# Performance work log

Measured on AMD Instinct MI355X. Metric: run time of the kernel, lower is better.

Reference implementation:

```python
import jax, jax.numpy as jnp
import numpy as np

D = 16          # u_emb_size
LAYER_NUM = 2   # CAN layer_num

def setup_inputs() -> dict:
    key = jax.random.key(0)
    k1, k2 = jax.random.split(key)
    B, N = 16384, 50
    user_emb = jax.random.normal(k1, (B, N, D), dtype=jnp.float32)
    # item side packs per-sample MLP params: [W0(d*d), b0(d), W1(d*d), b1(d)]
    item_emb = jax.random.normal(k2, (B, D * (D + 1) * LAYER_NUM), dtype=jnp.float32)
    return {"user_emb": user_emb, "item_emb": item_emb}

def reference(user_emb, item_emb):
    B = user_emb.shape[0]
    x = user_emb  # (B, N, D)
    off = 0
    for _ in range(LAYER_NUM):
        W = item_emb[:, off:off + D * D].reshape(B, D, D); off += D * D
        b = item_emb[:, off:off + D].reshape(B, 1, D);      off += D
        # per-sample batched matmul + bias + relu
        x = jax.nn.relu(jnp.einsum('bnd,bde->bne', x, W) + b)
    return x  # (B, N, D); is_seq=False, is_stacked=True -> return as-is
```

## Files before the change

kernel.cpp:

```cpp
#include <hip/hip_runtime.h>


#define CAN_D 16
#define CAN_N 50
#define CAN_PSTRIDE 544
#define WAVES_PER_BLOCK 4
#define YSTRIDE 20

typedef __attribute__((ext_vector_type(8))) short short8;
typedef __attribute__((ext_vector_type(4))) float f32x4;

union ABFrag { int i[4]; short8 v; };

__device__ __forceinline__ int pack2(float lo, float hi) {
    unsigned short ua = __builtin_bit_cast(unsigned short, (__bf16)lo);
    unsigned short ub = __builtin_bit_cast(unsigned short, (__bf16)hi);
    return (int)((unsigned)ua | ((unsigned)ub << 16));
}

__global__ __launch_bounds__(256, 5) void can_kernel(
    const float* __restrict__ user_emb,
    const float* __restrict__ item_emb,
    float* __restrict__ out, int B)
{
    __shared__ __align__(16) float ybuf[WAVES_PER_BLOCK][2][16 * YSTRIDE];

    const int wave = threadIdx.x >> 6;
    const int lane = threadIdx.x & 63;
    const int s = blockIdx.x * WAVES_PER_BLOCK + wave;
    if (s >= B) return;

    const int n    = lane & 15;
    const int quad = lane >> 4;

    const float* __restrict__ P     = item_emb + (size_t)s * CAN_PSTRIDE;
    const float* __restrict__ xbase = user_emb + (size_t)s * (CAN_N * CAN_D);
    float* __restrict__ obase       = out      + (size_t)s * (CAN_N * CAN_D);

    float t0[8], t1[8];
    if (quad < 2) {
        const float* W0 = P + quad * 8 * CAN_D + n;
        const float* W1 = P + 272 + quad * 8 * CAN_D + n;
#pragma unroll
        for (int j = 0; j < 8; ++j) { t0[j] = W0[j * CAN_D]; t1[j] = W1[j * CAN_D]; }
    }
    const float b0v = P[256 + n];
    const float b1v = P[528 + n];

    float4 xu0[4], xu1[4];
#pragma unroll
    for (int t = 0; t < 4; ++t) {
        if (quad < 2) {
            int row = t * 16 + n;
            if (row > CAN_N - 1) row = CAN_N - 1;
            const float4* px = (const float4*)(xbase + row * CAN_D + quad * 8);
            xu0[t] = px[0];
            xu1[t] = px[1];
        }
    }

    ABFrag w0, w1;
    if (quad < 2) {
#pragma unroll
        for (int j = 0; j < 4; ++j) {
            w0.i[j] = pack2(t0[2 * j], t0[2 * j + 1]);
            w1.i[j] = pack2(t1[2 * j], t1[2 * j + 1]);
        }
    } else {
#pragma unroll
        for (int j = 0; j < 4; ++j) { w0.i[j] = 0; w1.i[j] = 0; }
    }

    ABFrag a0[4];
#pragma unroll
    for (int t = 0; t < 4; ++t) {
        if (quad < 2) {
            a0[t].i[0] = pack2(xu0[t].x, xu0[t].y);
            a0[t].i[1] = pack2(xu0[t].z, xu0[t].w);
            a0[t].i[2] = pack2(xu1[t].x, xu1[t].y);
            a0[t].i[3] = pack2(xu1[t].z, xu1[t].w);
        } else {
#pragma unroll
            for (int j = 0; j < 4; ++j) a0[t].i[j] = 0;
        }
    }

#pragma unroll
    for (int t = 0; t < 4; ++t) {
        float* yb = &ybuf[wave][t & 1][0];

        f32x4 c0 = {b0v, b0v, b0v, b0v};
        c0 = __builtin_amdgcn_mfma_f32_16x16x32_bf16(a0[t].v, w0.v, c0, 0, 0, 0);

#pragma unroll
        for (int r = 0; r < 4; ++r)
            yb[(quad * 4 + r) * YSTRIDE + n] = fmaxf(c0[r], 0.0f);

        ABFrag a1;
        if (quad < 2) {
            const float* pr = yb + n * YSTRIDE + quad * 8;
            float4 v0 = *(const float4*)pr;
            float4 v1 = *(const float4*)(pr + 4);
            a1.i[0] = pack2(v0.x, v0.y);
            a1.i[1] = pack2(v0.z, v0.w);
            a1.i[2] = pack2(v1.x, v1.y);
            a1.i[3] = pack2(v1.z, v1.w);
        } else {
#pragma unroll
            for (int j = 0; j < 4; ++j) a1.i[j] = 0;
        }

        f32x4 c1 = {b1v, b1v, b1v, b1v};
        c1 = __builtin_amdgcn_mfma_f32_16x16x32_bf16(a1.v, w1.v, c1, 0, 0, 0);

#pragma unroll
        for (int r = 0; r < 4; ++r)
            yb[(quad * 4 + r) * YSTRIDE + n] = fmaxf(c1[r], 0.0f);

        const int srow = lane >> 2;
        const int scol = lane & 3;
        float4 ov = *(const float4*)(yb + srow * YSTRIDE + scol * 4);
        const int grow = t * 16 + srow;
        if (grow < CAN_N)
            *(float4*)(obase + grow * CAN_D + scol * 4) = ov;
    }
}

extern "C" void kernel_launch(void* const* d_in, const int* in_sizes, int n_in,
                              void* d_out, int out_size, void* d_ws, size_t ws_size,
                              hipStream_t stream) {
    const float* user_emb = (const float*)d_in[0];
    const float* item_emb = (const float*)d_in[1];
    float* out = (float*)d_out;

    const int B = in_sizes[0] / (CAN_N * CAN_D);
    const int blocks = (B + WAVES_PER_BLOCK - 1) / WAVES_PER_BLOCK;
    can_kernel<<<blocks, 256, 0, stream>>>(user_emb, item_emb, out, B);
}
```

Measured before the change: 126.5 us.

## Stage inputs into LDS with global_load_lds DMA and store outputs directly

Each wave now bulk-copies its sample's user embedding and per-sample MLP parameters from global memory into LDS using global_load_lds, with fully coalesced 16-byte transfers. Operand fragments are then built from LDS instead of through strided per-lane global loads. The layer-1 output is written straight from MFMA accumulators to global memory as 4-byte stores, dropping the LDS transpose. This also reuses the x staging area as the intermediate buffer, which makes LDS use per block larger, adds a block-wide barrier, and leaves the output stores less coalesced.

```diff
diff --git a/kernel.cpp b/kernel.cpp
--- a/kernel.cpp
+++ b/kernel.cpp
@@ -5,10 +5,15 @@
 #define CAN_N 50
 #define CAN_PSTRIDE 544
 #define WAVES_PER_BLOCK 4
-#define YSTRIDE 20
+#define XSTAGE 3328
+#define PSTAGE 2304
+#define SSTAGE (XSTAGE + PSTAGE)
+#define YS 20
 
 typedef __attribute__((ext_vector_type(8))) short short8;
 typedef __attribute__((ext_vector_type(4))) float f32x4;
+#define AS1 __attribute__((address_space(1)))
+#define AS3 __attribute__((address_space(3)))
 
 union ABFrag { int i[4]; short8 v; };
 
@@ -18,49 +23,60 @@
     return (int)((unsigned)ua | ((unsigned)ub << 16));
 }
 
+__device__ __forceinline__ void dma16(const float* g, char* l) {
+    __builtin_amdgcn_global_load_lds((const AS1 void*)g, (AS3 void*)l, 16, 0, 0);
+}
+__device__ __forceinline__ void dma4(const float* g, char* l) {
+    __builtin_amdgcn_global_load_lds((const AS1 void*)g, (AS3 void*)l, 4, 0, 0);
+}
+
 __global__ __launch_bounds__(256, 5) void can_kernel(
     const float* __restrict__ user_emb,
     const float* __restrict__ item_emb,
     float* __restrict__ out, int B)
 {
-    __shared__ __align__(16) float ybuf[WAVES_PER_BLOCK][2][16 * YSTRIDE];
+    __shared__ __align__(16) char smem[WAVES_PER_BLOCK * SSTAGE];
 
     const int wave = threadIdx.x >> 6;
     const int lane = threadIdx.x & 63;
     const int s = blockIdx.x * WAVES_PER_BLOCK + wave;
-    if (s >= B) return;
+    const bool active = (s < B);
+
+    char* xw = smem + wave * SSTAGE;
+    char* pw = xw + XSTAGE;
+
+    if (active) {
+        const float* gx = user_emb + (size_t)s * (CAN_N * CAN_D);
+        const float* gp = item_emb + (size_t)s * CAN_PSTRIDE;
+        dma16(gx +       lane * 4, xw);
+        dma16(gx + 256 + lane * 4, xw + 1024);
+        dma16(gx + 512 + lane * 4, xw + 2048);
+        { int idx = 768 + lane; if (idx > 799) idx = 799;
+          dma4(gx + idx, xw + 3072); }
+        dma16(gp +       lane * 4, pw);
+        dma16(gp + 256 + lane * 4, pw + 1024);
+        { int idx = 512 + lane; if (idx > 543) idx = 543;
+          dma4(gp + idx, pw + 2048); }
+    }
+
+    __syncthreads();
+    if (!active) return;
 
     const int n    = lane & 15;
     const int quad = lane >> 4;
-
-    const float* __restrict__ P     = item_emb + (size_t)s * CAN_PSTRIDE;
-    const float* __restrict__ xbase = user_emb + (size_t)s * (CAN_N * CAN_D);
-    float* __restrict__ obase       = out      + (size_t)s * (CAN_N * CAN_D);
-
-    float t0[8], t1[8];
-    if (quad < 2) {
-        const float* W0 = P + quad * 8 * CAN_D + n;
-        const float* W1 = P + 272 + quad * 8 * CAN_D + n;
-#pragma unroll
-        for (int j = 0; j < 8; ++j) { t0[j] = W0[j * CAN_D]; t1[j] = W1[j * CAN_D]; }
-    }
-    const float b0v = P[256 + n];
-    const float b1v = P[528 + n];
-
-    float4 xu0[4], xu1[4];
-#pragma unroll
-    for (int t = 0; t < 4; ++t) {
-        if (quad < 2) {
-            int row = t * 16 + n;
-            if (row > CAN_N - 1) row = CAN_N - 1;
-            const float4* px = (const float4*)(xbase + row * CAN_D + quad * 8);
-            xu0[t] = px[0];
-            xu1[t] = px[1];
-        }
-    }
+    const float* pf = (const float*)pw;
+    const float* xf = (const float*)xw;
 
     ABFrag w0, w1;
+    const float b0v = pf[256 + n];
+    const float b1v = pf[528 + n];
     if (quad < 2) {
+        float t0[8], t1[8];
+#pragma unroll
+        for (int j = 0; j < 8; ++j) {
+            t0[j] = pf[(quad * 8 + j) * CAN_D + n];
+            t1[j] = pf[272 + (quad * 8 + j) * CAN_D + n];
+        }
 #pragma unroll
         for (int j = 0; j < 4; ++j) {
             w0.i[j] = pack2(t0[2 * j], t0[2 * j + 1]);
@@ -75,30 +91,36 @@
 #pragma unroll
     for (int t = 0; t < 4; ++t) {
         if (quad < 2) {
-            a0[t].i[0] = pack2(xu0[t].x, xu0[t].y);
-            a0[t].i[1] = pack2(xu0[t].z, xu0[t].w);
-            a0[t].i[2] = pack2(xu1[t].x, xu1[t].y);
-            a0[t].i[3] = pack2(xu1[t].z, xu1[t].w);
+            int row = t * 16 + n;
+            if (row > CAN_N - 1) row = CAN_N - 1;
+            const float4* pr = (const float4*)(xf + row * CAN_D + quad * 8);
+            float4 u0 = pr[0], u1 = pr[1];
+            a0[t].i[0] = pack2(u0.x, u0.y);
+            a0[t].i[1] = pack2(u0.z, u0.w);
+            a0[t].i[2] = pack2(u1.x, u1.y);
+            a0[t].i[3] = pack2(u1.z, u1.w);
         } else {
 #pragma unroll
             for (int j = 0; j < 4; ++j) a0[t].i[j] = 0;
         }
     }
 
+    float* ob = out + (size_t)s * (CAN_N * CAN_D);
+
 #pragma unroll
     for (int t = 0; t < 4; ++t) {
-        float* yb = &ybuf[wave][t & 1][0];
+        float* yt = (float*)(xw + (t & 1) * 1280);
 
         f32x4 c0 = {b0v, b0v, b0v, b0v};
         c0 = __builtin_amdgcn_mfma_f32_16x16x32_bf16(a0[t].v, w0.v, c0, 0, 0, 0);
 
 #pragma unroll
         for (int r = 0; r < 4; ++r)
-            yb[(quad * 4 + r) * YSTRIDE + n] = fmaxf(c0[r], 0.0f);
+            yt[(quad * 4 + r) * YS + n] = fmaxf(c0[r], 0.0f);
 
         ABFrag a1;
         if (quad < 2) {
-            const float* pr = yb + n * YSTRIDE + quad * 8;
+            const float* pr = yt + n * YS + quad * 8;
             float4 v0 = *(const float4*)pr;
             float4 v1 = *(const float4*)(pr + 4);
             a1.i[0] = pack2(v0.x, v0.y);
@@ -114,15 +136,11 @@
         c1 = __builtin_amdgcn_mfma_f32_16x16x32_bf16(a1.v, w1.v, c1, 0, 0, 0);
 
 #pragma unroll
-        for (int r = 0; r < 4; ++r)
-            yb[(quad * 4 + r) * YSTRIDE + n] = fmaxf(c1[r], 0.0f);
-
-        const int srow = lane >> 2;
-        const int scol = lane & 3;
-        float4 ov = *(const float4*)(yb + srow * YSTRIDE + scol * 4);
-        const int grow = t * 16 + srow;
-        if (grow < CAN_N)
-            *(float4*)(obase + grow * CAN_D + scol * 4) = ov;
+        for (int r = 0; r < 4; ++r) {
+            int grow = t * 16 + quad * 4 + r;
+            if (grow < CAN_N)
+                ob[grow * CAN_D + n] = fmaxf(c1[r], 0.0f);
+        }
     }
 }
 
```

Result: faster. 124.0 us (-2.0%).

## Transpose MFMA operands and exchange layer activations via ds_bpermute instead of LDS

Applied to the files above, without the earlier changes.

Swaps the A/B operands of the MFMA so each lane's accumulator holds four consecutive output features for one row. Layer-0 results are packed to bf16 and redistributed across lanes with ds_bpermute, removing the shared-memory staging buffer and its store/load round trips. Final outputs are written straight from registers as float4 stores, and biases load as float4. Occupancy hint drops from 5 to 4 blocks, and the user-embedding loads are now interleaved with packing instead of issued all up front, which may reduce memory-level parallelism.

```diff
diff --git a/kernel.cpp b/kernel.cpp
--- a/kernel.cpp
+++ b/kernel.cpp
@@ -5,7 +5,6 @@
 #define CAN_N 50
 #define CAN_PSTRIDE 544
 #define WAVES_PER_BLOCK 4
-#define YSTRIDE 20
 
 typedef __attribute__((ext_vector_type(8))) short short8;
 typedef __attribute__((ext_vector_type(4))) float f32x4;
@@ -18,49 +17,31 @@
     return (int)((unsigned)ua | ((unsigned)ub << 16));
 }
 
-__global__ __launch_bounds__(256, 5) void can_kernel(
+__global__ __launch_bounds__(256, 4) void can_kernel(
     const float* __restrict__ user_emb,
     const float* __restrict__ item_emb,
     float* __restrict__ out, int B)
 {
-    __shared__ __align__(16) float ybuf[WAVES_PER_BLOCK][2][16 * YSTRIDE];
-
     const int wave = threadIdx.x >> 6;
     const int lane = threadIdx.x & 63;
     const int s = blockIdx.x * WAVES_PER_BLOCK + wave;
     if (s >= B) return;
 
-    const int n    = lane & 15;
+    const int e    = lane & 15;
     const int quad = lane >> 4;
 
-    const float* __restrict__ P     = item_emb + (size_t)s * CAN_PSTRIDE;
-    const float* __restrict__ xbase = user_emb + (size_t)s * (CAN_N * CAN_D);
-    float* __restrict__ obase       = out      + (size_t)s * (CAN_N * CAN_D);
-
-    float t0[8], t1[8];
-    if (quad < 2) {
-        const float* W0 = P + quad * 8 * CAN_D + n;
-        const float* W1 = P + 272 + quad * 8 * CAN_D + n;
-#pragma unroll
-        for (int j = 0; j < 8; ++j) { t0[j] = W0[j * CAN_D]; t1[j] = W1[j * CAN_D]; }
-    }
-    const float b0v = P[256 + n];
-    const float b1v = P[528 + n];
-
-    float4 xu0[4], xu1[4];
-#pragma unroll
-    for (int t = 0; t < 4; ++t) {
-        if (quad < 2) {
-            int row = t * 16 + n;
-            if (row > CAN_N - 1) row = CAN_N - 1;
-            const float4* px = (const float4*)(xbase + row * CAN_D + quad * 8);
-            xu0[t] = px[0];
-            xu1[t] = px[1];
-        }
-    }
+    const float* __restrict__ P  = item_emb + (size_t)s * CAN_PSTRIDE;
+    const float* __restrict__ xb = user_emb + (size_t)s * (CAN_N * CAN_D);
+    float* __restrict__ ob       = out      + (size_t)s * (CAN_N * CAN_D);
 
     ABFrag w0, w1;
     if (quad < 2) {
+        float t0[8], t1[8];
+#pragma unroll
+        for (int j = 0; j < 8; ++j) {
+            t0[j] = P[(quad * 8 + j) * CAN_D + e];
+            t1[j] = P[272 + (quad * 8 + j) * CAN_D + e];
+        }
 #pragma unroll
         for (int j = 0; j < 4; ++j) {
             w0.i[j] = pack2(t0[2 * j], t0[2 * j + 1]);
@@ -71,58 +52,57 @@
         for (int j = 0; j < 4; ++j) { w0.i[j] = 0; w1.i[j] = 0; }
     }
 
-    ABFrag a0[4];
+    const float4 b0q = *(const float4*)(P + 256 + 4 * quad);
+    const float4 b1q = *(const float4*)(P + 528 + 4 * quad);
+
+    ABFrag xf[4];
 #pragma unroll
     for (int t = 0; t < 4; ++t) {
         if (quad < 2) {
-            a0[t].i[0] = pack2(xu0[t].x, xu0[t].y);
-            a0[t].i[1] = pack2(xu0[t].z, xu0[t].w);
-            a0[t].i[2] = pack2(xu1[t].x, xu1[t].y);
-            a0[t].i[3] = pack2(xu1[t].z, xu1[t].w);
+            int row = t * 16 + e;
+            if (row > CAN_N - 1) row = CAN_N - 1;
+            const float4* pr = (const float4*)(xb + row * CAN_D + quad * 8);
+            float4 u0 = pr[0], u1 = pr[1];
+            xf[t].i[0] = pack2(u0.x, u0.y);
+            xf[t].i[1] = pack2(u0.z, u0.w);
+            xf[t].i[2] = pack2(u1.x, u1.y);
+            xf[t].i[3] = pack2(u1.z, u1.w);
         } else {
 #pragma unroll
-            for (int j = 0; j < 4; ++j) a0[t].i[j] = 0;
+            for (int j = 0; j < 4; ++j) xf[t].i[j] = 0;
         }
     }
 
+    const int addrA = ((lane & 15) + (quad & 1) * 32) * 4;
+    const int addrB = addrA + 64;
+
 #pragma unroll
     for (int t = 0; t < 4; ++t) {
-        float* yb = &ybuf[wave][t & 1][0];
+        f32x4 c = {b0q.x, b0q.y, b0q.z, b0q.w};
+        c = __builtin_amdgcn_mfma_f32_16x16x32_bf16(w0.v, xf[t].v, c, 0, 0, 0);
 
-        f32x4 c0 = {b0v, b0v, b0v, b0v};
-        c0 = __builtin_amdgcn_mfma_f32_16x16x32_bf16(a0[t].v, w0.v, c0, 0, 0, 0);
-
-#pragma unroll
-        for (int r = 0; r < 4; ++r)
-            yb[(quad * 4 + r) * YSTRIDE + n] = fmaxf(c0[r], 0.0f);
+        const int p0 = pack2(fmaxf(c[0], 0.f), fmaxf(c[1], 0.f));
+        const int p1 = pack2(fmaxf(c[2], 0.f), fmaxf(c[3], 0.f));
 
         ABFrag a1;
-        if (quad < 2) {
-            const float* pr = yb + n * YSTRIDE + quad * 8;
-            float4 v0 = *(const float4*)pr;
-            float4 v1 = *(const float4*)(pr + 4);
-            a1.i[0] = pack2(v0.x, v0.y);
-            a1.i[1] = pack2(v0.z, v0.w);
-            a1.i[2] = pack2(v1.x, v1.y);
-            a1.i[3] = pack2(v1.z, v1.w);
-        } else {
+        a1.i[0] = __builtin_amdgcn_ds_bpermute(addrA, p0);
+        a1.i[1] = __builtin_amdgcn_ds_bpermute(addrA, p1);
+        a1.i[2] = __builtin_amdgcn_ds_bpermute(addrB, p0);
+        a1.i[3] = __builtin_amdgcn_ds_bpermute(addrB, p1);
+        if (quad >= 2) {
 #pragma unroll
             for (int j = 0; j < 4; ++j) a1.i[j] = 0;
         }
 
-        f32x4 c1 = {b1v, b1v, b1v, b1v};
-        c1 = __builtin_amdgcn_mfma_f32_16x16x32_bf16(a1.v, w1.v, c1, 0, 0, 0);
+        f32x4 d = {b1q.x, b1q.y, b1q.z, b1q.w};
+        d = __builtin_amdgcn_mfma_f32_16x16x32_bf16(w1.v, a1.v, d, 0, 0, 0);
 
-#pragma unroll
-        for (int r = 0; r < 4; ++r)
-            yb[(quad * 4 + r) * YSTRIDE + n] = fmaxf(c1[r], 0.0f);
-
-        const int srow = lane >> 2;
-        const int scol = lane & 3;
-        float4 ov = *(const float4*)(yb + srow * YSTRIDE + scol * 4);
-        const int grow = t * 16 + srow;
-        if (grow < CAN_N)
-            *(float4*)(obase + grow * CAN_D + scol * 4) = ov;
+        const int grow = t * 16 + e;
+        if (grow < CAN_N) {
+            float4 ov = make_float4(fmaxf(d[0], 0.f), fmaxf(d[1], 0.f),
+                                    fmaxf(d[2], 0.f), fmaxf(d[3], 0.f));
+            *(float4*)(ob + grow * CAN_D + quad * 4) = ov;
+        }
     }
 }
 
```

Result: no change. 127.1 us (+0.5%).
